# Kernel tuning notes

Measured on AMD Instinct MI355X. Metric: run time of the kernel, lower is better.

## Reference

```python
import jax, jax.numpy as jnp
import numpy as np

N, E, H, NH, RBF_K = 512, 4096, 128, 8, 64
CUTOFF = 10.0
HH = H * NH  # 1024


def setup_inputs() -> dict:
    key = jax.random.key(0)
    ks = jax.random.split(key, 30)
    def lin_w(k, fan_in, fan_out):
        return jax.random.normal(k, (fan_in, fan_out), jnp.float32) * (fan_in ** -0.5)
    inp = {
        'atom_embs': jax.random.normal(ks[0], (N, H), jnp.float32),
        'pos': jax.random.normal(ks[1], (N, 3), jnp.float32),
        'edge_weight': jax.random.normal(ks[2], (E,), jnp.float32),
        'edge_indices': jax.random.randint(ks[3], (2, E), 0, N, jnp.int64),
        'Wq': lin_w(ks[4], H, HH),
        'Wk': lin_w(ks[5], H, HH),
        'Wv': lin_w(ks[6], H, HH),
        'li_w': lin_w(ks[7], H, H), 'li_b': jnp.zeros((H,), jnp.float32),
        'lj_w': lin_w(ks[8], H, H), 'lj_b': jnp.zeros((H,), jnp.float32),
        'el_w': lin_w(ks[9], 3 * H, HH), 'el_b': jnp.zeros((HH,), jnp.float32),
        'rl_w': lin_w(ks[10], RBF_K, HH), 'rl_b': jnp.zeros((HH,), jnp.float32),
        'ol_w': lin_w(ks[11], HH, H), 'ol_b': jnp.zeros((H,), jnp.float32),
        'ln_g': jnp.ones((H,), jnp.float32), 'ln_b': jnp.zeros((H,), jnp.float32),
        'f1_w': lin_w(ks[12], H, H), 'f1_b': jnp.zeros((H,), jnp.float32),
        'f2_w': lin_w(ks[13], H, H), 'f2_b': jnp.zeros((H,), jnp.float32),
        'f3_w': lin_w(ks[14], H, H), 'f3_b': jnp.zeros((H,), jnp.float32),
    }
    return inp


def _scatter_softmax_cols(logits, seg, num_segments):
    # softmax over columns of `logits` grouped by seg (column -> source node)
    lt = logits.T                                   # [E_cols, E_rows]
    m = jax.ops.segment_max(lt, seg, num_segments=num_segments)
    e = jnp.exp(lt - m[seg])
    s = jax.ops.segment_sum(e, seg, num_segments=num_segments)
    return (e / s[seg]).T


def _rbf(d):
    # d: [E, 1]. ExponentialRBF with softplus(softplus_inverse(x)) == x identities
    centers = jnp.linspace(1.0, np.exp(-CUTOFF).astype(np.float32), RBF_K)
    widths = np.float32((0.5 / ((1.0 - np.exp(-CUTOFF)) / RBF_K)) ** 2)
    x = d / CUTOFF
    x3 = x ** 3; x4 = x3 * x; x5 = x4 * x
    cut = jnp.where(x < 1, 1 - 6 * x5 + 15 * x4 - 10 * x3, jnp.zeros_like(x))
    return cut * jnp.exp(-widths * (jnp.exp(-d) - centers) ** 2)   # [E, K]


def reference(atom_embs, pos, edge_weight, edge_indices, Wq, Wk, Wv,
              li_w, li_b, lj_w, lj_b, el_w, el_b, rl_w, rl_b, ol_w, ol_b,
              ln_g, ln_b, f1_w, f1_b, f2_w, f2_b, f3_w, f3_b):
    src, tgt = edge_indices[0], edge_indices[1]
    ew = edge_weight[:, None]
    ai = atom_embs[tgt] + ew                      # atom_embs_i (+= edge_weight)
    aj = atom_embs[src] + ew                      # atom_embs_j (+= edge_weight)
    Q = ai @ Wq
    K = ai @ Wk
    V = ai @ Wv                                   # [E, HH]
    logits = (Q @ K.T) * (H ** -0.5)              # [E, E]
    prod = _scatter_softmax_cols(logits, src, N)  # scatter_softmax over edge_indices[0]
    hi = ai @ li_w + li_b
    hj = aj @ lj_w + lj_b
    edge_ij = jnp.concatenate([hi + hj, hi - hj, hi * hj], axis=-1)  # [E, 3H]
    d = jnp.linalg.norm(pos[tgt] - pos[src], axis=-1)[:, None]       # [E, 1]
    feats = edge_ij @ el_w + el_b + _rbf(d) @ rl_w + rl_b + V        # [E, HH]
    msg = (prod @ feats) @ ol_w + ol_b            # [E, H]
    agg = jax.ops.segment_sum(msg, tgt, num_segments=N)              # [N, H]

    def ln(x):
        mu = jnp.mean(x, -1, keepdims=True)
        var = jnp.var(x, -1, keepdims=True)
        return (x - mu) / jnp.sqrt(var + 1e-5) * ln_g + ln_b

    h = ln(agg)
    sp = jax.nn.softplus
    h = sp(sp(sp(h @ f1_w + f1_b) @ f2_w + f2_b) @ f3_w + f3_b)
    return ln(h)
```

## Files before the change

### kernel.cpp

```cpp
#include <hip/hip_runtime.h>
#include <math.h>

#define N_NODES 512
#define NE      4096
#define H       128
#define HH      1024
#define RBFK    64
#define KCAT    576

typedef __attribute__((ext_vector_type(8))) short bf16x8;
typedef __attribute__((ext_vector_type(4))) float f32x4;
typedef __attribute__((ext_vector_type(4))) short short4v;

__device__ __forceinline__ short f2bf(float x) {
    unsigned u = __builtin_bit_cast(unsigned, x);
    unsigned r = u + 0x7FFFu + ((u >> 16) & 1u);
    return (short)(r >> 16);
}
__device__ __forceinline__ float bf2f(short s) {
    return __builtin_bit_cast(float, ((unsigned)(unsigned short)s) << 16);
}

__device__ __forceinline__ void gload16(const short* g, short* l) {
    __builtin_amdgcn_global_load_lds(
        (const __attribute__((address_space(1))) void*)g,
        (__attribute__((address_space(3))) void*)l, 16, 0, 0);
}


__global__ __launch_bounds__(512) void k_scan(
    const int* __restrict__ ei,
    int* __restrict__ srcG, int* __restrict__ tgtG,
    int* __restrict__ segStart, int* __restrict__ segStartT,
    int* __restrict__ cursorS, int* __restrict__ cursorT, int* __restrict__ nsegp,
    float* __restrict__ cvec)
{
    __shared__ int hS[N_NODES], hT[N_NODES], sS[N_NODES], sT[N_NODES];
    __shared__ int flag;
    int t = threadIdx.x;
    if (t == 0) {
        int any = 0;
        for (int i = 1; i < 128; i += 2) any |= ei[i];
        flag = (any == 0);
    }
    hS[t] = 0; hT[t] = 0;
    if (t < H) cvec[t] = 0.0f;
    __syncthreads();
    int is64 = flag;
    for (int e = t; e < NE; e += 512) {
        int s = is64 ? ei[2 * e]          : ei[e];
        int g = is64 ? ei[2 * NE + 2 * e] : ei[NE + e];
        srcG[e] = s; tgtG[e] = g;
        atomicAdd(&hS[s], 1);
        atomicAdd(&hT[g], 1);
    }
    __syncthreads();
    int cs = hS[t], ct = hT[t];
    sS[t] = cs; sT[t] = ct;
    __syncthreads();
    for (int off = 1; off < N_NODES; off <<= 1) {
        int a = (t >= off) ? sS[t - off] : 0;
        int b = (t >= off) ? sT[t - off] : 0;
        __syncthreads();
        sS[t] += a; sT[t] += b;
        __syncthreads();
    }
    segStart[t + 1]  = sS[t];
    segStartT[t + 1] = sT[t];
    if (t == 0) { segStart[0] = 0; segStartT[0] = 0; }
    cursorS[t] = sS[t] - cs;
    cursorT[t] = sT[t] - ct;
    hS[t] = (cs > 0) ? 1 : 0;
    __syncthreads();
    for (int off = 256; off > 0; off >>= 1) {
        if (t < off) hS[t] += hS[t + off];
        __syncthreads();
    }
    if (t == 0) nsegp[0] = hS[0];
}

__global__ void k_scatter(const int* __restrict__ src, const int* __restrict__ tgt,
                          const float* __restrict__ ew,
                          int* __restrict__ cursorS, int* __restrict__ cursorT,
                          int* __restrict__ srcS, int* __restrict__ tgtS,
                          float* __restrict__ ewS, int* __restrict__ idxT) {
    int e = blockIdx.x * blockDim.x + threadIdx.x;
    if (e < NE) {
        int s = src[e], g = tgt[e];
        int p = atomicAdd(&cursorS[s], 1);
        srcS[p] = s; tgtS[p] = g; ewS[p] = ew[e];
        int q = atomicAdd(&cursorT[g], 1);
        idxT[q] = p;
    }
}

#define RA 524288
#define RB 589824
#define RBZ 65536
#define RQ 131072
#define RK 131072
#define RD 131072
#define RE 32768
#define RG 65536
#define RF 4096
#define RTOT (RA+RB+RBZ+RQ+RK+RD+RE+RG+RF)

__global__ void k_prep_all(
    const float* __restrict__ atom_embs, const float* __restrict__ pos,
    const int* __restrict__ srcS, const int* __restrict__ tgtS, const float* __restrict__ ewS,
    const float* __restrict__ Wq, const float* __restrict__ Wk, const float* __restrict__ Wv,
    const float* __restrict__ li_w, const float* __restrict__ lj_w,
    const float* __restrict__ el_w, const float* __restrict__ rl_w,
    const float* __restrict__ ol_w, const float* __restrict__ el_b, const float* __restrict__ rl_b,
    short* __restrict__ Acat, short* __restrict__ ajB, short* __restrict__ BcatT,
    short* __restrict__ WqB, short* __restrict__ WkB, short* __restrict__ olT,
    short* __restrict__ liT, short* __restrict__ ljT, short* __restrict__ embB,
    float* __restrict__ cvec)
{
    int idx = blockIdx.x * blockDim.x + threadIdx.x;
    if (idx < RA) {
        int p = idx >> 7, h = idx & 127;
        int s = srcS[p], t = tgtS[p];
        float ew = ewS[p];
        Acat[(size_t)p * KCAT + h] = f2bf(atom_embs[t * H + h] + ew);
        ajB[idx] = f2bf(atom_embs[s * H + h] + ew);
        if (h < RBFK) {
            float dx = pos[t * 3 + 0] - pos[s * 3 + 0];
            float dy = pos[t * 3 + 1] - pos[s * 3 + 1];
            float dz = pos[t * 3 + 2] - pos[s * 3 + 2];
            float d = sqrtf(dx * dx + dy * dy + dz * dz);
            float x = d * 0.1f;
            float cut = 0.0f;
            if (x < 1.0f) {
                float x3 = x * x * x, x4 = x3 * x, x5 = x4 * x;
                cut = 1.0f - 6.0f * x5 + 15.0f * x4 - 10.0f * x3;
            }
            float ck = 1.0f + (float)h * (-0.015872295239210119f);
            float tt = expf(-d) - ck;
            Acat[(size_t)p * KCAT + 512 + h] = f2bf(cut * expf(-1024.0929857f * tt * tt));
        }
        return;
    }
    idx -= RA;
    if (idx < RB) {
        int k = idx >> 10, n = idx & 1023;
        float v = (k < 128) ? Wv[k * HH + n]
                : (k < 512) ? el_w[(k - 128) * HH + n]
                            : rl_w[(k - 512) * HH + n];
        BcatT[idx] = f2bf(v);
        return;
    }
    idx -= RB;
    if (idx < RBZ) { BcatT[RB + idx] = 0; return; }
    idx -= RBZ;
    if (idx < RQ) { WqB[idx] = f2bf(Wq[idx]); return; }
    idx -= RQ;
    if (idx < RK) { WkB[idx] = f2bf(Wk[idx]); return; }
    idx -= RK;
    if (idx < RD) {
        int h = idx >> 10, n = idx & 1023;
        olT[idx] = f2bf(ol_w[n * H + h]);
        return;
    }
    idx -= RD;
    if (idx < RE) {
        int which = idx >> 14, r = idx & 16383;
        int n = r >> 7, k = r & 127;
        (which ? ljT : liT)[r] = f2bf((which ? lj_w : li_w)[k * H + n]);
        return;
    }
    idx -= RE;
    if (idx < RG) { embB[idx] = f2bf(atom_embs[idx]); return; }
    idx -= RG;
    if (idx < RF) {
        int h = idx & 127, chunk = idx >> 7;
        float acc = 0.0f;
        int n0 = chunk * 32;
        for (int n = n0; n < n0 + 32; n++)
            acc += (el_b[n] + rl_b[n]) * ol_w[n * H + h];
        atomicAdd(&cvec[h], acc);
    }
}

__device__ __forceinline__ void gemm_body(
    short* As, short* Bs,
    const short* __restrict__ A, int lda,
    const short* __restrict__ B, int ldb,
    void* __restrict__ Cp, int ldc,
    int kbeg, int kend, float alpha, const float* __restrict__ bias,
    long zoff_pitch, int out_mode, int row0, int col0)
{
    const int tid = threadIdx.x;
    const int wave = tid >> 6, lane = tid & 63;

    f32x4 acc[4][4];
#pragma unroll
    for (int i = 0; i < 4; i++)
#pragma unroll
        for (int j = 0; j < 4; j++) acc[i][j] = (f32x4){0.f, 0.f, 0.f, 0.f};

    const int m0 = (wave >> 1) * 64, n0 = (wave & 1) * 64;
    const int lr = lane >> 3;
    const int lc = (lane & 7) * 8;
    const int cl = lane & 15, quad = lane >> 4;

    for (int k0 = kbeg; k0 < kend; k0 += 64) {
#pragma unroll
        for (int i = 0; i < 4; i++) {
            int r = wave * 32 + i * 8;
            gload16(A + (size_t)(row0 + r + lr) * lda + k0 + lc, As + r * 64);
            gload16(B + (size_t)(col0 + r + lr) * ldb + k0 + lc, Bs + r * 64);
        }
        __syncthreads();
#pragma unroll
        for (int kk = 0; kk < 64; kk += 32) {
            bf16x8 af[4], bf[4];
            int ko = kk + quad * 8;
#pragma unroll
            for (int i = 0; i < 4; i++)
                af[i] = *(const bf16x8*)(As + (m0 + i * 16 + cl) * 64 + ko);
#pragma unroll
            for (int j = 0; j < 4; j++)
                bf[j] = *(const bf16x8*)(Bs + (n0 + j * 16 + cl) * 64 + ko);
#pragma unroll
            for (int i = 0; i < 4; i++)
#pragma unroll
                for (int j = 0; j < 4; j++)
                    acc[i][j] = __builtin_amdgcn_mfma_f32_16x16x32_bf16(af[i], bf[j], acc[i][j], 0, 0, 0);
        }
        __syncthreads();
    }

    if (out_mode == 1) {
        short* C = (short*)Cp;
#pragma unroll
        for (int i = 0; i < 4; i++)
#pragma unroll
            for (int j = 0; j < 4; j++) {
                int cc = col0 + n0 + j * 16 + cl;
                float bv = bias ? bias[cc] : 0.0f;
#pragma unroll
                for (int reg = 0; reg < 4; reg++) {
                    int rr = row0 + m0 + i * 16 + quad * 4 + reg;
                    C[(size_t)rr * ldc + cc] = f2bf(acc[i][j][reg] * alpha + bv);
                }
            }
    } else if (out_mode == 3) {
        short* C = (short*)Cp;
#pragma unroll
        for (int i = 0; i < 4; i++)
#pragma unroll
            for (int j = 0; j < 4; j++) {
                int cc = col0 + n0 + j * 16 + cl;
                int rr = row0 + m0 + i * 16 + quad * 4;
                short4v pack;
#pragma unroll
                for (int reg = 0; reg < 4; reg++) pack[reg] = f2bf(acc[i][j][reg] * alpha);
                *(short4v*)(C + (size_t)cc * ldc + rr) = pack;
            }
    } else {
        float* C = (float*)Cp + zoff_pitch;
#pragma unroll
        for (int i = 0; i < 4; i++)
#pragma unroll
            for (int j = 0; j < 4; j++) {
                int cc = col0 + n0 + j * 16 + cl;
#pragma unroll
                for (int reg = 0; reg < 4; reg++) {
                    int rr = row0 + m0 + i * 16 + quad * 4 + reg;
                    C[(size_t)rr * ldc + cc] = acc[i][j][reg] * alpha;
                }
            }
    }
}

__global__ __launch_bounds__(256) void k_gemm(
    const short* __restrict__ A, int lda,
    const short* __restrict__ B, int ldb,
    void* __restrict__ Cp, int ldc,
    int K, float alpha, const float* __restrict__ bias,
    long split_pitch, int out_mode)
{
    __shared__ __align__(16) short As[128 * 64];
    __shared__ __align__(16) short Bs[128 * 64];
    int kchunk = K / gridDim.z;
    gemm_body(As, Bs, A, lda, B, ldb, Cp, ldc,
              kchunk * blockIdx.z, kchunk * (blockIdx.z + 1), alpha, bias,
              (long)blockIdx.z * split_pitch, out_mode,
              blockIdx.y * 128, blockIdx.x * 128);
}

__global__ __launch_bounds__(256) void k_smallgemms(
    const short* __restrict__ olT, const short* __restrict__ BcatT,
    const short* __restrict__ WqB, const short* __restrict__ WkB,
    short* __restrict__ W2T, short* __restrict__ MT)
{
    __shared__ __align__(16) short As[128 * 64];
    __shared__ __align__(16) short Bs[128 * 64];
    if (blockIdx.x < 5) {
        gemm_body(As, Bs, olT, HH, BcatT, HH, W2T, 640, 0, HH, 1.0f, nullptr, 0, 1,
                  0, blockIdx.x * 128);
    } else {
        gemm_body(As, Bs, WqB, HH, WkB, HH, MT, 128, 0, HH, 1.0f, nullptr, 0, 3, 0, 0);
    }
}

__global__ __launch_bounds__(256) void k_midgemms(
    const short* __restrict__ Acat, const short* __restrict__ W2T,
    const short* __restrict__ MT, const short* __restrict__ embB,
    short* __restrict__ GT, short* __restrict__ Y)
{
    __shared__ __align__(16) short As[128 * 64];
    __shared__ __align__(16) short Bs[128 * 64];
    if (blockIdx.x < 32) {
        gemm_body(As, Bs, Acat, KCAT, W2T, 640, GT, NE, 0, KCAT, 1.0f, nullptr, 0, 3,
                  blockIdx.x * 128, 0);
    } else {
        gemm_body(As, Bs, embB, H, MT, H, Y, H, 0, H, 1.0f, nullptr, 0, 1,
                  (blockIdx.x - 32) * 128, 0);
    }
}

__global__ __launch_bounds__(256) void k_zgemm(
    const short* __restrict__ Y, const short* __restrict__ embB,
    const short* __restrict__ MT, const int* __restrict__ tgtS,
    const float* __restrict__ ewS,
    float* __restrict__ Z, float* __restrict__ pv,
    float* __restrict__ colP, float* __restrict__ colB)
{
    const float alpha = 0.08838834764831845f;
    __shared__ __align__(16) short As[128 * 64];
    __shared__ __align__(16) short Bs[128 * 64];
    if (blockIdx.x < 16) {
        gemm_body(As, Bs, Y, H, embB, H, Z, N_NODES, 0, H, alpha, nullptr, 0, 0,
                  (blockIdx.x >> 2) * 128, (blockIdx.x & 3) * 128);
    } else {
        __shared__ float csM[H];
        __shared__ float qsh[N_NODES];
        __shared__ float sSh;
        int t = threadIdx.x;
        if (t < H) {
            float a = 0.0f;
            for (int i = 0; i < H; i++) a += bf2f(MT[t * H + i]);
            csM[t] = a;
        }
        __syncthreads();
        for (int n = t; n < N_NODES; n += 256) {
            float a = 0.0f, b = 0.0f;
            for (int k = 0; k < H; k++) {
                a += bf2f(Y[n * H + k]);
                b += csM[k] * bf2f(embB[n * H + k]);
            }
            pv[n] = a; qsh[n] = b;
        }
        if (t == 0) {
            float s = 0.0f;
            for (int k = 0; k < H; k++) s += csM[k];
            sSh = s;
        }
        __syncthreads();
        float s = sSh;
        for (int c = t; c < NE; c += 256) {
            float ec = ewS[c];
            colP[c] = alpha * ec;
            colB[c] = alpha * (qsh[tgtS[c]] + ec * s);
        }
    }
}

__global__ __launch_bounds__(256) void k_edgefeat(
    const short* __restrict__ Acat_in, const short* __restrict__ ajB,
    const short* __restrict__ liT, const short* __restrict__ ljT,
    const float* __restrict__ li_b, const float* __restrict__ lj_b,
    short* __restrict__ Acat)
{
    __shared__ __align__(16) short As[128 * 128];
    __shared__ __align__(16) short Bs[128 * 128];
    const int tid = threadIdx.x;
    const int wave = tid >> 6, lane = tid & 63;
    const int row0 = blockIdx.x * 128;
    const int cl = lane & 15, quad = lane >> 4;
    const int m0 = (wave >> 1) * 64, n0 = (wave & 1) * 64;
    const int sr = lane >> 4, sc = (lane & 15) * 8;

    f32x4 ai_acc[4][4], aj_acc[4][4];
#pragma unroll
    for (int i = 0; i < 4; i++)
#pragma unroll
        for (int j = 0; j < 4; j++) {
            ai_acc[i][j] = (f32x4){0.f, 0.f, 0.f, 0.f};
            aj_acc[i][j] = (f32x4){0.f, 0.f, 0.f, 0.f};
        }

#pragma unroll
    for (int i = 0; i < 8; i++) {
        int r = wave * 32 + i * 4;
        gload16(Acat_in + (size_t)(row0 + r + sr) * KCAT + sc, As + r * 128);
        gload16(liT + (r + sr) * 128 + sc, Bs + r * 128);
    }
    __syncthreads();
#pragma unroll
    for (int kk = 0; kk < 128; kk += 32) {
        bf16x8 af[4], bf[4];
        int ko = kk + quad * 8;
#pragma unroll
        for (int i = 0; i < 4; i++) af[i] = *(const bf16x8*)(As + (m0 + i * 16 + cl) * 128 + ko);
#pragma unroll
        for (int j = 0; j < 4; j++) bf[j] = *(const bf16x8*)(Bs + (n0 + j * 16 + cl) * 128 + ko);
#pragma unroll
        for (int i = 0; i < 4; i++)
#pragma unroll
            for (int j = 0; j < 4; j++)
                ai_acc[i][j] = __builtin_amdgcn_mfma_f32_16x16x32_bf16(af[i], bf[j], ai_acc[i][j], 0, 0, 0);
    }
    __syncthreads();
#pragma unroll
    for (int i = 0; i < 8; i++) {
        int r = wave * 32 + i * 4;
        gload16(ajB + (size_t)(row0 + r + sr) * 128 + sc, As + r * 128);
        gload16(ljT + (r + sr) * 128 + sc, Bs + r * 128);
    }
    __syncthreads();
#pragma unroll
    for (int kk = 0; kk < 128; kk += 32) {
        bf16x8 af[4], bf[4];
        int ko = kk + quad * 8;
#pragma unroll
        for (int i = 0; i < 4; i++) af[i] = *(const bf16x8*)(As + (m0 + i * 16 + cl) * 128 + ko);
#pragma unroll
        for (int j = 0; j < 4; j++) bf[j] = *(const bf16x8*)(Bs + (n0 + j * 16 + cl) * 128 + ko);
#pragma unroll
        for (int i = 0; i < 4; i++)
#pragma unroll
            for (int j = 0; j < 4; j++)
                aj_acc[i][j] = __builtin_amdgcn_mfma_f32_16x16x32_bf16(af[i], bf[j], aj_acc[i][j], 0, 0, 0);
    }
#pragma unroll
    for (int i = 0; i < 4; i++)
#pragma unroll
        for (int j = 0; j < 4; j++) {
            int cc = n0 + j * 16 + cl;
            float bi = li_b[cc], bj = lj_b[cc];
#pragma unroll
            for (int reg = 0; reg < 4; reg++) {
                int rr = row0 + m0 + i * 16 + quad * 4 + reg;
                float hv = ai_acc[i][j][reg] + bi;
                float gv = aj_acc[i][j][reg] + bj;
                short* rowp = Acat + (size_t)rr * KCAT;
                rowp[128 + cc] = f2bf(hv + gv);
                rowp[256 + cc] = f2bf(hv - gv);
                rowp[384 + cc] = f2bf(hv * gv);
            }
        }
}

__global__ __launch_bounds__(512) void k_denom(
    const float* __restrict__ Z, const float* __restrict__ pv,
    const float* __restrict__ colP, const float* __restrict__ colB,
    const int* __restrict__ tgtS, const float* __restrict__ ewS,
    const int* __restrict__ segStart, float* __restrict__ rDen)
{
    __shared__ float row[NE];
    __shared__ float zrow[N_NODES];
    const int r = blockIdx.x, t = threadIdx.x;
    const int tr = tgtS[r];
    const float er = ewS[r];
    for (int i = t; i < N_NODES; i += 512)
        zrow[i] = Z[(size_t)tr * N_NODES + i];
    __syncthreads();
    const float p_tr = pv[tr];
    for (int c = t; c < NE; c += 512)
        row[c] = __expf(zrow[tgtS[c]] + colP[c] * p_tr + er * colB[c]);
    __syncthreads();
    float* rd = rDen + (size_t)r * N_NODES;
    if (t < N_NODES) {
        int a = segStart[t], b = segStart[t + 1];
        float s = 0.0f;
        for (int p = a; p < b; p++) s += row[p];
        rd[t] = (s > 0.0f) ? 1.0f / s : 0.0f;
    }
}

__global__ __launch_bounds__(256) void k_pagg2(
    const float* __restrict__ Z, const float* __restrict__ pv,
    const float* __restrict__ colP, const float* __restrict__ colB,
    const float* __restrict__ rDen,
    const int* __restrict__ tgtS, const float* __restrict__ ewS,
    const int* __restrict__ srcS, const int* __restrict__ segStartT,
    const int* __restrict__ idxT, short* __restrict__ PaggB)
{
    __shared__ float zrow[N_NODES];
    __shared__ float erL[32];
    __shared__ int   eL[32];
    const int n = blockIdx.y;
    const int c0 = blockIdx.x * 1024;
    const int t = threadIdx.x;
    for (int i = t; i < N_NODES; i += 256)
        zrow[i] = Z[(size_t)n * N_NODES + i];
    __syncthreads();
    const float p_n = pv[n];
    float A4[4], cB4[4];
    int sc4[4];
#pragma unroll
    for (int q = 0; q < 4; q++) {
        int c = c0 + t + q * 256;
        A4[q]  = zrow[tgtS[c]] + colP[c] * p_n;
        cB4[q] = colB[c];
        sc4[q] = srcS[c];
    }
    float acc[4] = {0.f, 0.f, 0.f, 0.f};
    const int a = segStartT[n], b = segStartT[n + 1];
    for (int ch = a; ch < b; ch += 32) {
        int ne = b - ch; if (ne > 32) ne = 32;
        __syncthreads();
        if (t < ne) { int e = idxT[ch + t]; eL[t] = e; erL[t] = ewS[e]; }
        __syncthreads();
        for (int k = 0; k < ne; k++) {
            const float er = erL[k];
            const float* rde = rDen + (size_t)eL[k] * N_NODES;
#pragma unroll
            for (int q = 0; q < 4; q++)
                acc[q] += __expf(A4[q] + er * cB4[q]) * rde[sc4[q]];
        }
    }
    short* pr = PaggB + (size_t)n * NE + c0;
#pragma unroll
    for (int q = 0; q < 4; q++)
        pr[t + q * 256] = f2bf(acc[q]);
}

__global__ __launch_bounds__(128) void k_head(
    const float* __restrict__ aggP, const int* __restrict__ segStartT,
    const int* __restrict__ nsegp,
    const float* __restrict__ cvec, const float* __restrict__ ol_b,
    const float* __restrict__ ln_g, const float* __restrict__ ln_b,
    const float* __restrict__ f1_w, const float* __restrict__ f1_b,
    const float* __restrict__ f2_w, const float* __restrict__ f2_b,
    const float* __restrict__ f3_w, const float* __restrict__ f3_b,
    float* __restrict__ out)
{
    __shared__ float x[H];
    __shared__ float red[H];
    int t = threadIdx.x, row = blockIdx.x;
    int cnt = segStartT[row + 1] - segStartT[row];
    float v = (float)cnt * (ol_b[t] + (float)nsegp[0] * cvec[t]);
    const float* ap = aggP + (size_t)row * H + t;
#pragma unroll
    for (int z = 0; z < 8; z++) v += ap[(size_t)z * N_NODES * H];
    red[t] = v; __syncthreads();
    for (int s = 64; s > 0; s >>= 1) { if (t < s) red[t] += red[t + s]; __syncthreads(); }
    float mu = red[0] * (1.0f / H); __syncthreads();
    float dv = v - mu;
    red[t] = dv * dv; __syncthreads();
    for (int s = 64; s > 0; s >>= 1) { if (t < s) red[t] += red[t + s]; __syncthreads(); }
    float var = red[0] * (1.0f / H); __syncthreads();
    x[t] = dv * rsqrtf(var + 1e-5f) * ln_g[t] + ln_b[t];
    __syncthreads();
    const float* Ws[3] = { f1_w, f2_w, f3_w };
    const float* Bb[3] = { f1_b, f2_b, f3_b };
    for (int l = 0; l < 3; l++) {
        float acc = Bb[l][t];
        const float* Wl = Ws[l];
        for (int k = 0; k < H; k++) acc = fmaf(x[k], Wl[k * H + t], acc);
        float o = fmaxf(acc, 0.0f) + log1pf(expf(-fabsf(acc)));
        __syncthreads();
        x[t] = o;
        __syncthreads();
    }
    float xv = x[t];
    red[t] = xv; __syncthreads();
    for (int s = 64; s > 0; s >>= 1) { if (t < s) red[t] += red[t + s]; __syncthreads(); }
    mu = red[0] * (1.0f / H); __syncthreads();
    float dv2 = xv - mu;
    red[t] = dv2 * dv2; __syncthreads();
    for (int s = 64; s > 0; s >>= 1) { if (t < s) red[t] += red[t + s]; __syncthreads(); }
    var = red[0] * (1.0f / H);
    out[row * H + t] = dv2 * rsqrtf(var + 1e-5f) * ln_g[t] + ln_b[t];
}


extern "C" void kernel_launch(void* const* d_in, const int* in_sizes, int n_in,
                              void* d_out, int out_size, void* d_ws, size_t ws_size,
                              hipStream_t stream) {
    const float* atom_embs   = (const float*)d_in[0];
    const float* pos         = (const float*)d_in[1];
    const float* edge_weight = (const float*)d_in[2];
    const int*   edge_idx    = (const int*)d_in[3];
    const float* Wq   = (const float*)d_in[4];
    const float* Wk   = (const float*)d_in[5];
    const float* Wv   = (const float*)d_in[6];
    const float* li_w = (const float*)d_in[7];
    const float* li_b = (const float*)d_in[8];
    const float* lj_w = (const float*)d_in[9];
    const float* lj_b = (const float*)d_in[10];
    const float* el_w = (const float*)d_in[11];
    const float* el_b = (const float*)d_in[12];
    const float* rl_w = (const float*)d_in[13];
    const float* rl_b = (const float*)d_in[14];
    const float* ol_w = (const float*)d_in[15];
    const float* ol_b = (const float*)d_in[16];
    const float* ln_g = (const float*)d_in[17];
    const float* ln_b = (const float*)d_in[18];
    const float* f1_w = (const float*)d_in[19];
    const float* f1_b = (const float*)d_in[20];
    const float* f2_w = (const float*)d_in[21];
    const float* f2_b = (const float*)d_in[22];
    const float* f3_w = (const float*)d_in[23];
    const float* f3_b = (const float*)d_in[24];
    float* out = (float*)d_out;

    char* w = (char*)d_ws;
    size_t off = 0;
    auto alloc = [&](size_t bytes) -> void* {
        void* p = w + off;
        off += (bytes + 255) & ~(size_t)255;
        return p;
    };
    int*   src       = (int*)alloc(NE * 4);
    int*   tgt       = (int*)alloc(NE * 4);
    int*   srcS      = (int*)alloc(NE * 4);
    int*   tgtS      = (int*)alloc(NE * 4);
    float* ewS       = (float*)alloc(NE * 4);
    int*   segStart  = (int*)alloc((N_NODES + 1) * 4);
    int*   segStartT = (int*)alloc((N_NODES + 1) * 4);
    int*   cursorS   = (int*)alloc(N_NODES * 4);
    int*   cursorT   = (int*)alloc(N_NODES * 4);
    int*   idxT      = (int*)alloc(NE * 4);
    int*   nsegp     = (int*)alloc(4);
    short* Acat   = (short*)alloc((size_t)NE * KCAT * 2);
    short* ajB    = (short*)alloc((size_t)NE * H * 2);
    short* BcatT  = (short*)alloc((size_t)640 * HH * 2);
    short* WqB    = (short*)alloc((size_t)H * HH * 2);
    short* WkB    = (short*)alloc((size_t)H * HH * 2);
    short* olT    = (short*)alloc((size_t)H * HH * 2);
    short* liT    = (short*)alloc((size_t)H * H * 2);
    short* ljT    = (short*)alloc((size_t)H * H * 2);
    short* embB   = (short*)alloc((size_t)N_NODES * H * 2);
    float* cvec   = (float*)alloc(H * 4);
    short* W2T    = (short*)alloc((size_t)H * 640 * 2);
    short* MT     = (short*)alloc((size_t)H * H * 2);
    short* Y      = (short*)alloc((size_t)N_NODES * H * 2);
    float* Z      = (float*)alloc((size_t)N_NODES * N_NODES * 4);
    float* pv     = (float*)alloc(N_NODES * 4);
    float* colP   = (float*)alloc(NE * 4);
    float* colB   = (float*)alloc(NE * 4);
    short* GT     = (short*)alloc((size_t)H * NE * 2);
    float* rDen   = (float*)alloc((size_t)NE * N_NODES * 4);
    short* PaggB  = (short*)alloc((size_t)N_NODES * NE * 2);
    float* aggP   = (float*)alloc((size_t)8 * N_NODES * H * 4);

    k_scan<<<1, 512, 0, stream>>>(edge_idx, src, tgt, segStart, segStartT,
                                  cursorS, cursorT, nsegp, cvec);
    k_scatter<<<NE / 256, 256, 0, stream>>>(src, tgt, edge_weight, cursorS, cursorT,
                                            srcS, tgtS, ewS, idxT);
    k_prep_all<<<(RTOT + 255) / 256, 256, 0, stream>>>(
        atom_embs, pos, srcS, tgtS, ewS,
        Wq, Wk, Wv, li_w, lj_w, el_w, rl_w, ol_w, el_b, rl_b,
        Acat, ajB, BcatT, WqB, WkB, olT, liT, ljT, embB, cvec);
    k_edgefeat<<<NE / 128, 256, 0, stream>>>(Acat, ajB, liT, ljT, li_b, lj_b, Acat);

    k_smallgemms<<<6, 256, 0, stream>>>(olT, BcatT, WqB, WkB, W2T, MT);
    k_midgemms<<<36, 256, 0, stream>>>(Acat, W2T, MT, embB, GT, Y);
    k_zgemm<<<17, 256, 0, stream>>>(Y, embB, MT, tgtS, ewS, Z, pv, colP, colB);

    k_denom<<<NE, 512, 0, stream>>>(Z, pv, colP, colB, tgtS, ewS, segStart, rDen);
    {
        dim3 g(4, N_NODES);
        k_pagg2<<<g, 256, 0, stream>>>(Z, pv, colP, colB, rDen, tgtS, ewS, srcS,
                                       segStartT, idxT, PaggB);
    }
    {
        dim3 g(1, N_NODES / 128, 8);
        k_gemm<<<g, 256, 0, stream>>>(PaggB, NE, GT, NE, aggP, H, NE, 1.0f, nullptr,
                                      (long)N_NODES * H, 0);
    }
    k_head<<<N_NODES, 128, 0, stream>>>(aggP, segStartT, nsegp, cvec, ol_b,
                                        ln_g, ln_b, f1_w, f1_b, f2_w, f2_b, f3_w, f3_b, out);
}
```

Baseline: 241.4 us.

## Merge edge-feature, QK projection and W2 GEMMs into fewer launches, reorder Z computation

Replaces the Wq·Wk^T fold (MT) path with direct projection of node embeddings into Q and K, computing Z as Q·K^T over K=1024, and uses column sums of Wq/Wk for the bias terms. Edge-feature, QK projection and W2 GEMMs are combined into one launch, and the GT GEMM is merged with the softmax denominator kernel, so launches and serialized small kernels are reduced. The cost is a larger Z GEMM (K=1024 instead of 128) and a serial per-thread 1024-length loop in the column-bias block.

```diff
diff --git a/kernel.cpp b/kernel.cpp
--- a/kernel.cpp
+++ b/kernel.cpp
@@ -97,13 +97,13 @@
 #define RA 524288
 #define RB 589824
 #define RBZ 65536
-#define RQ 131072
-#define RK 131072
+#define RW 262144
+#define RCW 2048
 #define RD 131072
 #define RE 32768
 #define RG 65536
 #define RF 4096
-#define RTOT (RA+RB+RBZ+RQ+RK+RD+RE+RG+RF)
+#define RTOT (RA+RB+RBZ+RW+RCW+RD+RE+RG+RF)
 
 __global__ void k_prep_all(
     const float* __restrict__ atom_embs, const float* __restrict__ pos,
@@ -113,9 +113,9 @@
     const float* __restrict__ el_w, const float* __restrict__ rl_w,
     const float* __restrict__ ol_w, const float* __restrict__ el_b, const float* __restrict__ rl_b,
     short* __restrict__ Acat, short* __restrict__ ajB, short* __restrict__ BcatT,
-    short* __restrict__ WqB, short* __restrict__ WkB, short* __restrict__ olT,
-    short* __restrict__ liT, short* __restrict__ ljT, short* __restrict__ embB,
-    float* __restrict__ cvec)
+    short* __restrict__ WqkT, float* __restrict__ cwq, float* __restrict__ cwk,
+    short* __restrict__ olT, short* __restrict__ liT, short* __restrict__ ljT,
+    short* __restrict__ embB, float* __restrict__ cvec)
 {
     int idx = blockIdx.x * blockDim.x + threadIdx.x;
     if (idx < RA) {
@@ -153,10 +153,22 @@
     idx -= RB;
     if (idx < RBZ) { BcatT[RB + idx] = 0; return; }
     idx -= RBZ;
-    if (idx < RQ) { WqB[idx] = f2bf(Wq[idx]); return; }
-    idx -= RQ;
-    if (idx < RK) { WkB[idx] = f2bf(Wk[idx]); return; }
-    idx -= RK;
+    if (idx < RW) {
+        int n = idx >> 7, k = idx & 127;
+        float v = (n < 1024) ? Wq[k * HH + n] : Wk[k * HH + (n - 1024)];
+        WqkT[idx] = f2bf(v);
+        return;
+    }
+    idx -= RW;
+    if (idx < RCW) {
+        int which = idx >> 10, j = idx & 1023;
+        const float* W = which ? Wk : Wq;
+        float s = 0.0f;
+        for (int k = 0; k < H; k++) s += W[k * HH + j];
+        (which ? cwk : cwq)[j] = s;
+        return;
+    }
+    idx -= RCW;
     if (idx < RD) {
         int h = idx >> 10, n = idx & 1023;
         olT[idx] = f2bf(ol_w[n * H + h]);
@@ -290,95 +302,15 @@
               blockIdx.y * 128, blockIdx.x * 128);
 }
 
-__global__ __launch_bounds__(256) void k_smallgemms(
-    const short* __restrict__ olT, const short* __restrict__ BcatT,
-    const short* __restrict__ WqB, const short* __restrict__ WkB,
-    short* __restrict__ W2T, short* __restrict__ MT)
-{
-    __shared__ __align__(16) short As[128 * 64];
-    __shared__ __align__(16) short Bs[128 * 64];
-    if (blockIdx.x < 5) {
-        gemm_body(As, Bs, olT, HH, BcatT, HH, W2T, 640, 0, HH, 1.0f, nullptr, 0, 1,
-                  0, blockIdx.x * 128);
-    } else {
-        gemm_body(As, Bs, WqB, HH, WkB, HH, MT, 128, 0, HH, 1.0f, nullptr, 0, 3, 0, 0);
-    }
-}
-
-__global__ __launch_bounds__(256) void k_midgemms(
-    const short* __restrict__ Acat, const short* __restrict__ W2T,
-    const short* __restrict__ MT, const short* __restrict__ embB,
-    short* __restrict__ GT, short* __restrict__ Y)
-{
-    __shared__ __align__(16) short As[128 * 64];
-    __shared__ __align__(16) short Bs[128 * 64];
-    if (blockIdx.x < 32) {
-        gemm_body(As, Bs, Acat, KCAT, W2T, 640, GT, NE, 0, KCAT, 1.0f, nullptr, 0, 3,
-                  blockIdx.x * 128, 0);
-    } else {
-        gemm_body(As, Bs, embB, H, MT, H, Y, H, 0, H, 1.0f, nullptr, 0, 1,
-                  (blockIdx.x - 32) * 128, 0);
-    }
-}
-
-__global__ __launch_bounds__(256) void k_zgemm(
-    const short* __restrict__ Y, const short* __restrict__ embB,
-    const short* __restrict__ MT, const int* __restrict__ tgtS,
-    const float* __restrict__ ewS,
-    float* __restrict__ Z, float* __restrict__ pv,
-    float* __restrict__ colP, float* __restrict__ colB)
-{
-    const float alpha = 0.08838834764831845f;
-    __shared__ __align__(16) short As[128 * 64];
-    __shared__ __align__(16) short Bs[128 * 64];
-    if (blockIdx.x < 16) {
-        gemm_body(As, Bs, Y, H, embB, H, Z, N_NODES, 0, H, alpha, nullptr, 0, 0,
-                  (blockIdx.x >> 2) * 128, (blockIdx.x & 3) * 128);
-    } else {
-        __shared__ float csM[H];
-        __shared__ float qsh[N_NODES];
-        __shared__ float sSh;
-        int t = threadIdx.x;
-        if (t < H) {
-            float a = 0.0f;
-            for (int i = 0; i < H; i++) a += bf2f(MT[t * H + i]);
-            csM[t] = a;
-        }
-        __syncthreads();
-        for (int n = t; n < N_NODES; n += 256) {
-            float a = 0.0f, b = 0.0f;
-            for (int k = 0; k < H; k++) {
-                a += bf2f(Y[n * H + k]);
-                b += csM[k] * bf2f(embB[n * H + k]);
-            }
-            pv[n] = a; qsh[n] = b;
-        }
-        if (t == 0) {
-            float s = 0.0f;
-            for (int k = 0; k < H; k++) s += csM[k];
-            sSh = s;
-        }
-        __syncthreads();
-        float s = sSh;
-        for (int c = t; c < NE; c += 256) {
-            float ec = ewS[c];
-            colP[c] = alpha * ec;
-            colB[c] = alpha * (qsh[tgtS[c]] + ec * s);
-        }
-    }
-}
-
-__global__ __launch_bounds__(256) void k_edgefeat(
+__device__ __forceinline__ void edgefeat_body(
+    short* As, short* Bs, int row0,
     const short* __restrict__ Acat_in, const short* __restrict__ ajB,
     const short* __restrict__ liT, const short* __restrict__ ljT,
     const float* __restrict__ li_b, const float* __restrict__ lj_b,
     short* __restrict__ Acat)
 {
-    __shared__ __align__(16) short As[128 * 128];
-    __shared__ __align__(16) short Bs[128 * 128];
     const int tid = threadIdx.x;
     const int wave = tid >> 6, lane = tid & 63;
-    const int row0 = blockIdx.x * 128;
     const int cl = lane & 15, quad = lane >> 4;
     const int m0 = (wave >> 1) * 64, n0 = (wave & 1) * 64;
     const int sr = lane >> 4, sc = (lane & 15) * 8;
@@ -454,30 +386,107 @@
         }
 }
 
-__global__ __launch_bounds__(512) void k_denom(
+__global__ __launch_bounds__(256) void k_big(
+    const short* __restrict__ Acat_in, const short* __restrict__ ajB,
+    const short* __restrict__ liT, const short* __restrict__ ljT,
+    const float* __restrict__ li_b, const float* __restrict__ lj_b,
+    short* __restrict__ Acat,
+    const short* __restrict__ embB, const short* __restrict__ WqkT,
+    short* __restrict__ QKB,
+    const short* __restrict__ olT, const short* __restrict__ BcatT,
+    short* __restrict__ W2T)
+{
+    __shared__ __align__(16) char smem[65536];
+    if (blockIdx.x < 32) {
+        edgefeat_body((short*)smem, (short*)(smem + 32768), blockIdx.x * 128,
+                      Acat_in, ajB, liT, ljT, li_b, lj_b, Acat);
+    } else if (blockIdx.x < 96) {
+        int id = blockIdx.x - 32;
+        gemm_body((short*)smem, (short*)(smem + 16384),
+                  embB, H, WqkT, H, QKB, 2048, 0, H, 1.0f, nullptr, 0, 1,
+                  (id >> 4) * 128, (id & 15) * 128);
+    } else {
+        int id = blockIdx.x - 96;
+        gemm_body((short*)smem, (short*)(smem + 16384),
+                  olT, HH, BcatT, HH, W2T, 640, 0, HH, 1.0f, nullptr, 0, 1,
+                  0, id * 128);
+    }
+}
+
+__global__ __launch_bounds__(256) void k_zr(
+    const short* __restrict__ QKB,
+    const float* __restrict__ cwq, const float* __restrict__ cwk,
+    const int* __restrict__ tgtS, const float* __restrict__ ewS,
+    float* __restrict__ Z, float* __restrict__ pv,
+    float* __restrict__ colP, float* __restrict__ colB)
+{
+    const float alpha = 0.08838834764831845f;
+    __shared__ __align__(16) char smem[32768];
+    if (blockIdx.x < 16) {
+        gemm_body((short*)smem, (short*)(smem + 16384),
+                  QKB, 2048, QKB + 1024, 2048, Z, N_NODES, 0, HH, alpha, nullptr, 0, 0,
+                  (blockIdx.x >> 2) * 128, (blockIdx.x & 3) * 128);
+    } else {
+        float* qsh = (float*)smem;
+        __shared__ float sSh;
+        int t = threadIdx.x;
+        for (int n = t; n < N_NODES; n += 256) {
+            const short* qr = QKB + (size_t)n * 2048;
+            float pa = 0.0f, qa = 0.0f;
+            for (int j = 0; j < HH; j++) {
+                pa += bf2f(qr[j]) * cwk[j];
+                qa += bf2f(qr[1024 + j]) * cwq[j];
+            }
+            pv[n] = pa; qsh[n] = qa;
+        }
+        if (t == 0) {
+            float s = 0.0f;
+            for (int j = 0; j < HH; j++) s += cwq[j] * cwk[j];
+            sSh = s;
+        }
+        __syncthreads();
+        float s = sSh;
+        for (int c = t; c < NE; c += 256) {
+            float ec = ewS[c];
+            colP[c] = alpha * ec;
+            colB[c] = alpha * (qsh[tgtS[c]] + ec * s);
+        }
+    }
+}
+
+__global__ __launch_bounds__(256) void k_denomgt(
+    const short* __restrict__ Acat, const short* __restrict__ W2T,
+    short* __restrict__ GT,
     const float* __restrict__ Z, const float* __restrict__ pv,
     const float* __restrict__ colP, const float* __restrict__ colB,
     const int* __restrict__ tgtS, const float* __restrict__ ewS,
     const int* __restrict__ segStart, float* __restrict__ rDen)
 {
-    __shared__ float row[NE];
-    __shared__ float zrow[N_NODES];
-    const int r = blockIdx.x, t = threadIdx.x;
+    __shared__ __align__(16) char smem[32768];
+    if (blockIdx.x < 32) {
+        gemm_body((short*)smem, (short*)(smem + 16384),
+                  Acat, KCAT, W2T, 640, GT, NE, 0, KCAT, 1.0f, nullptr, 0, 3,
+                  blockIdx.x * 128, 0);
+        return;
+    }
+    float* row  = (float*)smem;
+    float* zrow = (float*)(smem + 16384);
+    const int r = blockIdx.x - 32, t = threadIdx.x;
     const int tr = tgtS[r];
     const float er = ewS[r];
-    for (int i = t; i < N_NODES; i += 512)
+    for (int i = t; i < N_NODES; i += 256)
         zrow[i] = Z[(size_t)tr * N_NODES + i];
     __syncthreads();
     const float p_tr = pv[tr];
-    for (int c = t; c < NE; c += 512)
+    for (int c = t; c < NE; c += 256)
         row[c] = __expf(zrow[tgtS[c]] + colP[c] * p_tr + er * colB[c]);
     __syncthreads();
     float* rd = rDen + (size_t)r * N_NODES;
-    if (t < N_NODES) {
-        int a = segStart[t], b = segStart[t + 1];
+    for (int n = t; n < N_NODES; n += 256) {
+        int a = segStart[n], b = segStart[n + 1];
         float s = 0.0f;
         for (int p = a; p < b; p++) s += row[p];
-        rd[t] = (s > 0.0f) ? 1.0f / s : 0.0f;
+        rd[n] = (s > 0.0f) ? 1.0f / s : 0.0f;
     }
 }
 
@@ -630,16 +639,16 @@
     short* Acat   = (short*)alloc((size_t)NE * KCAT * 2);
     short* ajB    = (short*)alloc((size_t)NE * H * 2);
     short* BcatT  = (short*)alloc((size_t)640 * HH * 2);
-    short* WqB    = (short*)alloc((size_t)H * HH * 2);
-    short* WkB    = (short*)alloc((size_t)H * HH * 2);
+    short* WqkT   = (short*)alloc((size_t)2048 * H * 2);
+    float* cwq    = (float*)alloc(HH * 4);
+    float* cwk    = (float*)alloc(HH * 4);
     short* olT    = (short*)alloc((size_t)H * HH * 2);
     short* liT    = (short*)alloc((size_t)H * H * 2);
     short* ljT    = (short*)alloc((size_t)H * H * 2);
     short* embB   = (short*)alloc((size_t)N_NODES * H * 2);
     float* cvec   = (float*)alloc(H * 4);
     short* W2T    = (short*)alloc((size_t)H * 640 * 2);
-    short* MT     = (short*)alloc((size_t)H * H * 2);
-    short* Y      = (short*)alloc((size_t)N_NODES * H * 2);
+    short* QKB    = (short*)alloc((size_t)N_NODES * 2048 * 2);
     float* Z      = (float*)alloc((size_t)N_NODES * N_NODES * 4);
     float* pv     = (float*)alloc(N_NODES * 4);
     float* colP   = (float*)alloc(NE * 4);
@@ -656,14 +665,13 @@
     k_prep_all<<<(RTOT + 255) / 256, 256, 0, stream>>>(
         atom_embs, pos, srcS, tgtS, ewS,
         Wq, Wk, Wv, li_w, lj_w, el_w, rl_w, ol_w, el_b, rl_b,
-        Acat, ajB, BcatT, WqB, WkB, olT, liT, ljT, embB, cvec);
-    k_edgefeat<<<NE / 128, 256, 0, stream>>>(Acat, ajB, liT, ljT, li_b, lj_b, Acat);
-
-    k_smallgemms<<<6, 256, 0, stream>>>(olT, BcatT, WqB, WkB, W2T, MT);
-    k_midgemms<<<36, 256, 0, stream>>>(Acat, W2T, MT, embB, GT, Y);
-    k_zgemm<<<17, 256, 0, stream>>>(Y, embB, MT, tgtS, ewS, Z, pv, colP, colB);
-
-    k_denom<<<NE, 512, 0, stream>>>(Z, pv, colP, colB, tgtS, ewS, segStart, rDen);
+        Acat, ajB, BcatT, WqkT, cwq, cwk, olT, liT, ljT, embB, cvec);
+
+    k_big<<<101, 256, 0, stream>>>(Acat, ajB, liT, ljT, li_b, lj_b, Acat,
+                                   embB, WqkT, QKB, olT, BcatT, W2T);
+    k_zr<<<17, 256, 0, stream>>>(QKB, cwq, cwk, tgtS, ewS, Z, pv, colP, colB);
+    k_denomgt<<<32 + NE, 256, 0, stream>>>(Acat, W2T, GT, Z, pv, colP, colB,
+                                           tgtS, ewS, segStart, rDen);
     {
         dim3 g(4, N_NODES);
         k_pagg2<<<g, 256, 0, stream>>>(Z, pv, colP, colB, rDen, tgtS, ewS, srcS,
```

New measurement: 317.5 us. +31.5%, slower.
